# Performance work log

Hardware: AMD Instinct MI355X
Metric: run time of the kernel (lower is better)

## Reference

```python
import jax, jax.numpy as jnp
import numpy as np

VOCAB = 32000
MAXLEN = 512
E = 768
H = 12
D = E // H  # 64
L = 6
F = int(E * 8 / 3)  # 2048
THETA = 10000.0
EPS = 1.1920929e-07  # torch.finfo(float32).eps, RMSNorm default


def _rms_norm(x, w):
    var = jnp.mean(x * x, axis=-1, keepdims=True)
    return x * jax.lax.rsqrt(var + EPS) * w


def _rope(x, cos, sin):
    # x: [B,H,C,D]; cos/sin: [C,D/2] (interleaved even/odd convention)
    xe = x[..., 0::2]
    xo = x[..., 1::2]
    re = xe * cos - xo * sin
    ro = xe * sin + xo * cos
    out = jnp.stack([re, ro], axis=-1)  # [B,H,C,D/2,2]
    return out.reshape(x.shape)


def setup_inputs() -> dict:
    key = jax.random.key(0)
    ks = jax.random.split(key, 13)
    s = 0.02
    ids = jax.random.randint(ks[0], (8, MAXLEN), 0, VOCAB)
    embed = jax.random.normal(ks[1], (VOCAB, E), jnp.float32) * s
    norm1_w = jnp.ones((L, E), jnp.float32)
    wq = jax.random.normal(ks[2], (L, E, H * D), jnp.float32) * s
    wk = jax.random.normal(ks[3], (L, E, H * D), jnp.float32) * s
    wv = jax.random.normal(ks[4], (L, E, H * D), jnp.float32) * s
    wo = jax.random.normal(ks[5], (L, H * D, E), jnp.float32) * s
    norm2_w = jnp.ones((L, E), jnp.float32)
    w_gate = jax.random.normal(ks[6], (L, E, F), jnp.float32) * s
    w_val = jax.random.normal(ks[7], (L, E, F), jnp.float32) * s
    w_out = jax.random.normal(ks[8], (L, F, E), jnp.float32) * s
    normf_w = jnp.ones((E,), jnp.float32)
    unembed = jax.random.normal(ks[9], (E, VOCAB), jnp.float32) * s
    return {"ids": ids, "embed": embed, "norm1_w": norm1_w, "wq": wq,
            "wk": wk, "wv": wv, "wo": wo, "norm2_w": norm2_w,
            "w_gate": w_gate, "w_val": w_val, "w_out": w_out,
            "normf_w": normf_w, "unembed": unembed}


def reference(ids, embed, norm1_w, wq, wk, wv, wo, norm2_w,
              w_gate, w_val, w_out, normf_w, unembed):
    B, C = ids.shape
    # RoPE caches [C, D/2]
    half_ids = jnp.arange(D // 2, dtype=jnp.float32)
    inv_freq = 1.0 / (THETA ** (2.0 * half_ids / D))
    angles = jnp.arange(C, dtype=jnp.float32)[:, None] * inv_freq[None, :]
    cos, sin = jnp.cos(angles), jnp.sin(angles)
    causal = jnp.tril(jnp.ones((C, C), bool))

    x = embed[ids]  # [B,C,E]
    for l in range(L):
        h = _rms_norm(x, norm1_w[l])
        q = (h @ wq[l]).reshape(B, C, H, D).transpose(0, 2, 1, 3)
        k = (h @ wk[l]).reshape(B, C, H, D).transpose(0, 2, 1, 3)
        v = (h @ wv[l]).reshape(B, C, H, D).transpose(0, 2, 1, 3)
        q = _rope(q, cos, sin)
        k = _rope(k, cos, sin)
        scores = jnp.einsum('bhqd,bhkd->bhqk', q, k) / jnp.sqrt(jnp.float32(D))
        scores = jnp.where(causal, scores, -jnp.inf)
        w = jax.nn.softmax(scores, axis=-1)
        attn = jnp.einsum('bhqk,bhkd->bhqd', w, v)
        attn = attn.transpose(0, 2, 1, 3).reshape(B, C, H * D)
        x = x + attn @ wo[l]
        h2 = _rms_norm(x, norm2_w[l])
        gated = jax.nn.silu(h2 @ w_gate[l]) * (h2 @ w_val[l])
        x = x + gated @ w_out[l]
    x = _rms_norm(x, normf_w)
    return x @ unembed  # [B,C,VOCAB]
```

## Files before the change

kernel.cpp:

```cpp
#include <hip/hip_runtime.h>
#include <hip/hip_bf16.h>
#include <stdint.h>

typedef __hip_bfloat16 bf16;
typedef unsigned short ushort_t;
typedef __attribute__((ext_vector_type(8))) short bf16x8;
typedef __attribute__((ext_vector_type(4))) float f32x4;

#define EPSV 1.1920929e-07f

__device__ __forceinline__ float bfu2f(uint32_t u) {
  union { uint32_t i; float f; } t; t.i = u << 16; return t.f;
}
__device__ __forceinline__ ushort_t f2bfu(float f) {
  bf16 h = __float2bfloat16(f);
  return *reinterpret_cast<ushort_t*>(&h);
}

#define BAR() __builtin_amdgcn_s_barrier()
#define SCHEDB() __builtin_amdgcn_sched_barrier(0)
#define WAIT_LGKM0() { asm volatile("s_waitcnt lgkmcnt(0)" ::: "memory"); SCHEDB(); }
#define WAIT_VM4() asm volatile("s_waitcnt vmcnt(4)" ::: "memory")
#define WAIT_VM0() asm volatile("s_waitcnt vmcnt(0)" ::: "memory")

__global__ void rope_table_kernel(float* __restrict__ cosT, float* __restrict__ sinT) {
  int i = blockIdx.x * 256 + threadIdx.x;
  if (i >= 512 * 32) return;
  int c = i >> 5, dp = i & 31;
  float inv = powf(10000.0f, -(2.0f * dp) / 64.0f);
  float a = (float)c * inv;
  cosT[i] = cosf(a);
  sinT[i] = sinf(a);
}

__global__ void embed_kernel(const int* __restrict__ ids, const float* __restrict__ emb,
                             float* __restrict__ x) {
  int t = blockIdx.x;
  int id = ids[t];
  const float4* s = (const float4*)(emb + (size_t)id * 768);
  float4* d = (float4*)(x + (size_t)t * 768);
  d[threadIdx.x] = s[threadIdx.x];
}

__global__ __launch_bounds__(256) void rmsnorm_kernel(const float* __restrict__ x,
                                                      const float* __restrict__ wgt,
                                                      bf16* __restrict__ out) {
  const int row = blockIdx.x;
  const int tid = threadIdx.x;
  const float* xr = x + (size_t)row * 768;
  float v0 = xr[tid], v1 = xr[tid + 256], v2 = xr[tid + 512];
  float s = v0 * v0 + v1 * v1 + v2 * v2;
#pragma unroll
  for (int d = 1; d < 64; d <<= 1) s += __shfl_xor(s, d);
  __shared__ float red[4];
  if ((tid & 63) == 0) red[tid >> 6] = s;
  __syncthreads();
  s = red[0] + red[1] + red[2] + red[3];
  float rs = rsqrtf(s * (1.0f / 768.0f) + EPSV);
  bf16* orow = out + (size_t)row * 768;
  orow[tid]       = __float2bfloat16(v0 * rs * wgt[tid]);
  orow[tid + 256] = __float2bfloat16(v1 * rs * wgt[tid + 256]);
  orow[tid + 512] = __float2bfloat16(v2 * rs * wgt[tid + 512]);
}

__global__ __launch_bounds__(256) void transpose_kernel(const float* __restrict__ in,
                                                        bf16* __restrict__ out,
                                                        int K, int N) {
  __shared__ float tile[32][33];
  int nt = blockIdx.x * 32, kt = blockIdx.y * 32;
  int tx = threadIdx.x & 31, ty = threadIdx.x >> 5;
#pragma unroll
  for (int i = 0; i < 4; ++i)
    tile[ty + i * 8][tx] = in[(size_t)(kt + ty + i * 8) * N + nt + tx];
  __syncthreads();
#pragma unroll
  for (int i = 0; i < 4; ++i)
    out[(size_t)(nt + ty + i * 8) * K + kt + tx] = __float2bfloat16(tile[tx][ty + i * 8]);
}

template <int MODE>
__global__ __launch_bounds__(256) void gemm_bt(const bf16* __restrict__ A,
                                               const bf16* __restrict__ BT,
                                               void* __restrict__ C,
                                               int M, int N, int K) {
  __shared__ __align__(16) bf16 As[128 * 32];
  __shared__ __align__(16) bf16 Bs[128 * 32];
  const int tid = threadIdx.x;
  const int lane = tid & 63, w = tid >> 6;
  const int g = lane >> 4, lc = lane & 15;
  const int bm = blockIdx.y * 128, bn = blockIdx.x * 128;
  const int wm = (w >> 1) * 64, wn = (w & 1) * 64;

  f32x4 acc[4][4];
#pragma unroll
  for (int i = 0; i < 4; ++i)
#pragma unroll
    for (int j = 0; j < 4; ++j) acc[i][j] = (f32x4){0.f, 0.f, 0.f, 0.f};

  for (int k0 = 0; k0 < K; k0 += 32) {
    __syncthreads();
#pragma unroll
    for (int j = 0; j < 2; ++j) {
      int c = (w * 2 + j) * 64 + lane;
      int row = c >> 2, part = c & 3;
      const bf16* srcA = A + (size_t)(bm + row) * K + k0 + part * 8;
      const bf16* srcB = BT + (size_t)(bn + row) * K + k0 + part * 8;
      __builtin_amdgcn_global_load_lds((const __attribute__((address_space(1))) void*)srcA,
                                       (__attribute__((address_space(3))) void*)(As + (w * 2 + j) * 512),
                                       16, 0, 0);
      __builtin_amdgcn_global_load_lds((const __attribute__((address_space(1))) void*)srcB,
                                       (__attribute__((address_space(3))) void*)(Bs + (w * 2 + j) * 512),
                                       16, 0, 0);
    }
    __syncthreads();
    bf16x8 af[4], bfr[4];
#pragma unroll
    for (int mi = 0; mi < 4; ++mi)
      af[mi] = *(const bf16x8*)(As + (wm + mi * 16 + lc) * 32 + g * 8);
#pragma unroll
    for (int ni = 0; ni < 4; ++ni)
      bfr[ni] = *(const bf16x8*)(Bs + (wn + ni * 16 + lc) * 32 + g * 8);
#pragma unroll
    for (int mi = 0; mi < 4; ++mi)
#pragma unroll
      for (int ni = 0; ni < 4; ++ni)
        acc[mi][ni] = __builtin_amdgcn_mfma_f32_16x16x32_bf16(af[mi], bfr[ni], acc[mi][ni], 0, 0, 0);
  }

#pragma unroll
  for (int mi = 0; mi < 4; ++mi)
#pragma unroll
    for (int ni = 0; ni < 4; ++ni)
#pragma unroll
      for (int r = 0; r < 4; ++r) {
        size_t row = (size_t)bm + wm + mi * 16 + g * 4 + r;
        size_t col = (size_t)bn + wn + ni * 16 + lc;
        float v = acc[mi][ni][r];
        if (MODE == 0)      ((bf16*)C)[row * N + col] = __float2bfloat16(v);
        else if (MODE == 1) ((float*)C)[row * N + col] = v;
        else                ((float*)C)[row * N + col] += v;
      }
}

template <int MODE>
__global__ __launch_bounds__(512, 2) void gemm256(const bf16* __restrict__ A,
                                                  const bf16* __restrict__ BT,
                                                  void* __restrict__ C,
                                                  int M, int N, int K) {
  __shared__ __align__(16) bf16 lds[2][4][256 * 32];

  const int tid = threadIdx.x;
  const int lane = tid & 63, w = tid >> 6;
  const int wr = w >> 2, wc = w & 3;
  const int g = lane >> 4, lc = lane & 15;

  const int nwg = gridDim.x;
  const int q = nwg >> 3;
  const int wg = ((int)blockIdx.x & 7) * q + ((int)blockIdx.x >> 3);
  const int nby = M >> 8;
  const int bx = wg / nby, by = wg % nby;
  const int bm = by << 8, bn = bx << 8;

  const bf16* Ap = A + (size_t)bm * K;
  const bf16* Bp = BT + (size_t)bn * K;

  const int soff = (lc * 64) + ((((lane >> 4) ^ ((lane >> 1) & 3)) << 4));

  auto stage_half = [&](int buf, int slab, const bf16* Base, int kcol) {
#pragma unroll
    for (int j = 0; j < 2; ++j) {
      int half_id = w * 2 + j;
      int row = half_id * 16 + (lane >> 2);
      int s_log = (lane & 3) ^ ((lane >> 3) & 3);
      const bf16* src = Base + (size_t)row * K + kcol + s_log * 8;
      bf16* dst = &lds[buf][slab][half_id * 512];
      __builtin_amdgcn_global_load_lds((const __attribute__((address_space(1))) void*)src,
                                       (__attribute__((address_space(3))) void*)dst,
                                       16, 0, 0);
    }
  };

  f32x4 acc[8][4];
#pragma unroll
  for (int i = 0; i < 8; ++i)
#pragma unroll
    for (int j = 0; j < 4; ++j) acc[i][j] = (f32x4){0.f, 0.f, 0.f, 0.f};

  const int NT = K >> 6;

  stage_half(0, 0, Ap, 0);
  stage_half(0, 1, Bp, 0);
  stage_half(0, 2, Ap, 32);
  stage_half(0, 3, Bp, 32);

  bf16x8 aF[4], bF[4];

  auto ds_A = [&](int buf, int kk, int mh) {
#pragma unroll
    for (int i = 0; i < 4; ++i) {
      int byte = (wr * 128 + mh * 64 + i * 16) * 64 + soff;
      aF[i] = *(const bf16x8*)((const char*)&lds[buf][kk * 2][0] + byte);
    }
  };
  auto ds_B = [&](int buf, int kk) {
#pragma unroll
    for (int nf = 0; nf < 4; ++nf) {
      int byte = (wc * 64 + nf * 16) * 64 + soff;
      bF[nf] = *(const bf16x8*)((const char*)&lds[buf][kk * 2 + 1][0] + byte);
    }
  };
  auto mfma16 = [&](int mh) {
    __builtin_amdgcn_s_setprio(1);
#pragma unroll
    for (int i = 0; i < 4; ++i)
#pragma unroll
      for (int nf = 0; nf < 4; ++nf)
        acc[mh * 4 + i][nf] =
            __builtin_amdgcn_mfma_f32_16x16x32_bf16(aF[i], bF[nf], acc[mh * 4 + i][nf], 0, 0, 0);
    __builtin_amdgcn_s_setprio(0);
  };

  for (int t = 0; t < NT; ++t) {
    const int buf = t & 1;
    const bool pf = (t + 1) < NT;
    const int knext = (t + 1) << 6;

    WAIT_VM4();
    BAR(); SCHEDB();
    if (pf) stage_half(buf ^ 1, 0, Ap, knext);
    ds_A(buf, 0, 0);
    ds_B(buf, 0);
    BAR();
    WAIT_LGKM0();
    mfma16(0);
    if (pf) stage_half(buf ^ 1, 1, Bp, knext);
    ds_A(buf, 0, 1);
    BAR();
    WAIT_LGKM0();
    mfma16(1);
    if (pf) { WAIT_VM4(); } else { WAIT_VM0(); }
    BAR(); SCHEDB();
    if (pf) stage_half(buf ^ 1, 2, Ap, knext + 32);
    ds_A(buf, 1, 0);
    ds_B(buf, 1);
    BAR();
    WAIT_LGKM0();
    mfma16(0);
    if (pf) stage_half(buf ^ 1, 3, Bp, knext + 32);
    ds_A(buf, 1, 1);
    BAR();
    WAIT_LGKM0();
    mfma16(1);
  }

#pragma unroll
  for (int mf = 0; mf < 8; ++mf)
#pragma unroll
    for (int nf = 0; nf < 4; ++nf)
#pragma unroll
      for (int r = 0; r < 4; ++r) {
        size_t row = (size_t)bm + wr * 128 + mf * 16 + g * 4 + r;
        size_t col = (size_t)bn + wc * 64 + nf * 16 + lc;
        float v = acc[mf][nf][r];
        if (MODE == 0) ((bf16*)C)[row * N + col] = __float2bfloat16(v);
        else           ((float*)C)[row * N + col] = v;
      }
}

__global__ __launch_bounds__(256) void attn_kernel(const bf16* __restrict__ qkv,
                                                   const float* __restrict__ cosT,
                                                   const float* __restrict__ sinT,
                                                   bf16* __restrict__ out) {
  const int qt = blockIdx.x;
  const int h  = blockIdx.y;
  const int b  = blockIdx.z;
  const int tid = threadIdx.x;
  const int lane = tid & 63, w = tid >> 6;
  const int g = lane >> 4, lc = lane & 15;

  __shared__ __align__(16) bf16 Qs[128][72];
  __shared__ __align__(16) bf16 Ks[64][72];
  __shared__ __align__(16) bf16 Vt[64][72];
  __shared__ __align__(16) bf16 Pl[4][32][72];

  for (int i = 0; i < 16; ++i) {
    int pi = i * 256 + tid;
    int r = pi >> 5, dp = pi & 31;
    int c = qt * 128 + r;
    size_t t = (size_t)b * 512 + c;
    uint32_t u = *(const uint32_t*)(qkv + t * 2304 + h * 64 + dp * 2);
    float xe = bfu2f(u & 0xffffu), xo = bfu2f(u >> 16);
    float cs = cosT[c * 32 + dp], sn = sinT[c * 32 + dp];
    float re = (xe * cs - xo * sn) * 0.125f;
    float ro = (xe * sn + xo * cs) * 0.125f;
    *(uint32_t*)&Qs[r][dp * 2] = (uint32_t)f2bfu(re) | ((uint32_t)f2bfu(ro) << 16);
  }
  __syncthreads();
  bf16x8 qa[2][2];
#pragma unroll
  for (int mi = 0; mi < 2; ++mi)
#pragma unroll
    for (int ks = 0; ks < 2; ++ks)
      qa[mi][ks] = *(const bf16x8*)&Qs[w * 32 + mi * 16 + lc][ks * 32 + g * 8];

  float m_r[2][4], l_r[2][4];
  f32x4 acc_o[2][4];
#pragma unroll
  for (int mi = 0; mi < 2; ++mi)
#pragma unroll
    for (int r = 0; r < 4; ++r) { m_r[mi][r] = -1e30f; l_r[mi][r] = 0.f; }
#pragma unroll
  for (int mi = 0; mi < 2; ++mi)
#pragma unroll
    for (int ni = 0; ni < 4; ++ni) acc_o[mi][ni] = (f32x4){0.f, 0.f, 0.f, 0.f};

  const int nkt = 2 * qt + 2;
  for (int kt = 0; kt < nkt; ++kt) {
    __syncthreads();
    for (int i = 0; i < 8; ++i) {
      int pi = i * 256 + tid;
      int r = pi >> 5, dp = pi & 31;
      int c = kt * 64 + r;
      size_t t = (size_t)b * 512 + c;
      uint32_t u = *(const uint32_t*)(qkv + t * 2304 + 768 + h * 64 + dp * 2);
      float xe = bfu2f(u & 0xffffu), xo = bfu2f(u >> 16);
      float cs = cosT[c * 32 + dp], sn = sinT[c * 32 + dp];
      *(uint32_t*)&Ks[r][dp * 2] =
          (uint32_t)f2bfu(xe * cs - xo * sn) | ((uint32_t)f2bfu(xe * sn + xo * cs) << 16);
      uint32_t uv = *(const uint32_t*)(qkv + t * 2304 + 1536 + h * 64 + dp * 2);
      *(ushort_t*)&Vt[dp * 2][r]     = (ushort_t)(uv & 0xffffu);
      *(ushort_t*)&Vt[dp * 2 + 1][r] = (ushort_t)(uv >> 16);
    }
    __syncthreads();

    f32x4 sacc[2][4];
#pragma unroll
    for (int mi = 0; mi < 2; ++mi)
#pragma unroll
      for (int ni = 0; ni < 4; ++ni) sacc[mi][ni] = (f32x4){0.f, 0.f, 0.f, 0.f};
#pragma unroll
    for (int ni = 0; ni < 4; ++ni) {
      bf16x8 kb0 = *(const bf16x8*)&Ks[ni * 16 + lc][g * 8];
      bf16x8 kb1 = *(const bf16x8*)&Ks[ni * 16 + lc][32 + g * 8];
#pragma unroll
      for (int mi = 0; mi < 2; ++mi) {
        sacc[mi][ni] = __builtin_amdgcn_mfma_f32_16x16x32_bf16(qa[mi][0], kb0, sacc[mi][ni], 0, 0, 0);
        sacc[mi][ni] = __builtin_amdgcn_mfma_f32_16x16x32_bf16(qa[mi][1], kb1, sacc[mi][ni], 0, 0, 0);
      }
    }
    if (kt >= 2 * qt) {
#pragma unroll
      for (int mi = 0; mi < 2; ++mi)
#pragma unroll
        for (int ni = 0; ni < 4; ++ni)
#pragma unroll
          for (int r = 0; r < 4; ++r) {
            int ql = w * 32 + mi * 16 + g * 4 + r;
            int kl = ni * 16 + lc;
            if (kt * 64 + kl > qt * 128 + ql) sacc[mi][ni][r] = -1e30f;
          }
    }
#pragma unroll
    for (int mi = 0; mi < 2; ++mi) {
      float mx[4], sm[4], mn[4], sc[4];
#pragma unroll
      for (int r = 0; r < 4; ++r)
        mx[r] = fmaxf(fmaxf(sacc[mi][0][r], sacc[mi][1][r]), fmaxf(sacc[mi][2][r], sacc[mi][3][r]));
#pragma unroll
      for (int d = 1; d < 16; d <<= 1)
#pragma unroll
        for (int r = 0; r < 4; ++r) mx[r] = fmaxf(mx[r], __shfl_xor(mx[r], d));
#pragma unroll
      for (int r = 0; r < 4; ++r) {
        mn[r] = fmaxf(m_r[mi][r], mx[r]);
        sc[r] = __expf(m_r[mi][r] - mn[r]);
        sm[r] = 0.f;
      }
#pragma unroll
      for (int ni = 0; ni < 4; ++ni)
#pragma unroll
        for (int r = 0; r < 4; ++r) {
          float p = __expf(sacc[mi][ni][r] - mn[r]);
          sacc[mi][ni][r] = p;
          sm[r] += p;
        }
#pragma unroll
      for (int d = 1; d < 16; d <<= 1)
#pragma unroll
        for (int r = 0; r < 4; ++r) sm[r] += __shfl_xor(sm[r], d);
#pragma unroll
      for (int r = 0; r < 4; ++r) {
        l_r[mi][r] = l_r[mi][r] * sc[r] + sm[r];
        m_r[mi][r] = mn[r];
      }
#pragma unroll
      for (int ni = 0; ni < 4; ++ni)
#pragma unroll
        for (int r = 0; r < 4; ++r) acc_o[mi][ni][r] *= sc[r];
#pragma unroll
      for (int ni = 0; ni < 4; ++ni)
#pragma unroll
        for (int r = 0; r < 4; ++r)
          *(ushort_t*)&Pl[w][mi * 16 + g * 4 + r][ni * 16 + lc] = f2bfu(sacc[mi][ni][r]);
    }
    __syncthreads();
#pragma unroll
    for (int ks = 0; ks < 2; ++ks) {
      bf16x8 pa[2];
#pragma unroll
      for (int mi = 0; mi < 2; ++mi)
        pa[mi] = *(const bf16x8*)&Pl[w][mi * 16 + lc][ks * 32 + g * 8];
#pragma unroll
      for (int ni = 0; ni < 4; ++ni) {
        bf16x8 vb = *(const bf16x8*)&Vt[ni * 16 + lc][ks * 32 + g * 8];
#pragma unroll
        for (int mi = 0; mi < 2; ++mi)
          acc_o[mi][ni] = __builtin_amdgcn_mfma_f32_16x16x32_bf16(pa[mi], vb, acc_o[mi][ni], 0, 0, 0);
      }
    }
  }
#pragma unroll
  for (int mi = 0; mi < 2; ++mi) {
    float inv[4];
#pragma unroll
    for (int r = 0; r < 4; ++r) inv[r] = 1.0f / l_r[mi][r];
#pragma unroll
    for (int ni = 0; ni < 4; ++ni)
#pragma unroll
      for (int r = 0; r < 4; ++r) {
        size_t t = (size_t)b * 512 + qt * 128 + w * 32 + mi * 16 + g * 4 + r;
        int d = ni * 16 + lc;
        out[t * 768 + h * 64 + d] = __float2bfloat16(acc_o[mi][ni][r] * inv[r]);
      }
  }
}

__global__ void silu_mul_kernel(const float* __restrict__ gv, bf16* __restrict__ act) {
  size_t i = (size_t)blockIdx.x * 256 + threadIdx.x;
  int t = (int)(i >> 11);
  int j = (int)(i & 2047);
  float gval = gv[(size_t)t * 4096 + j];
  float vval = gv[(size_t)t * 4096 + 2048 + j];
  float sg = gval / (1.0f + __expf(-gval));
  act[i] = __float2bfloat16(sg * vval);
}

extern "C" void kernel_launch(void* const* d_in, const int* in_sizes, int n_in,
                              void* d_out, int out_size, void* d_ws, size_t ws_size,
                              hipStream_t stream) {
  const int*   ids    = (const int*)d_in[0];
  const float* embedW = (const float*)d_in[1];
  const float* norm1w = (const float*)d_in[2];
  const float* wq     = (const float*)d_in[3];
  const float* wk     = (const float*)d_in[4];
  const float* wv     = (const float*)d_in[5];
  const float* wo     = (const float*)d_in[6];
  const float* norm2w = (const float*)d_in[7];
  const float* wgate  = (const float*)d_in[8];
  const float* wval   = (const float*)d_in[9];
  const float* wout   = (const float*)d_in[10];
  const float* normfw = (const float*)d_in[11];
  const float* unemb  = (const float*)d_in[12];

  char* arena = (char*)d_out;
  size_t off = 0;
  auto alloc = [&](size_t bytes) -> char* {
    char* p = arena + off;
    off += (bytes + 255) & ~(size_t)255;
    return p;
  };
  float* x       = (float*)alloc(4096ull * 768 * 4);
  bf16*  h       = (bf16*)alloc(4096ull * 768 * 2);
  bf16*  qkv     = (bf16*)alloc(4096ull * 2304 * 2);
  bf16*  attnout = (bf16*)alloc(4096ull * 768 * 2);
  float* gv      = (float*)alloc(4096ull * 4096 * 4);
  bf16*  act     = (bf16*)alloc(4096ull * 2048 * 2);
  float* cosT    = (float*)alloc(512 * 32 * 4);
  float* sinT    = (float*)alloc(512 * 32 * 4);
  bf16*  wqkvT   = (bf16*)alloc(2304ull * 768 * 2);
  bf16*  woT     = (bf16*)alloc(768ull * 768 * 2);
  bf16*  wgvT    = (bf16*)alloc(4096ull * 768 * 2);
  bf16*  woutT   = (bf16*)alloc(768ull * 2048 * 2);

  bf16* unembT = (bf16*)d_ws;
  bf16* hf     = (bf16*)((char*)d_ws + 32000ull * 768 * 2);

  rope_table_kernel<<<64, 256, 0, stream>>>(cosT, sinT);
  embed_kernel<<<4096, 192, 0, stream>>>(ids, embedW, x);

  for (int l = 0; l < 6; ++l) {
    rmsnorm_kernel<<<4096, 256, 0, stream>>>(x, norm1w + (size_t)l * 768, h);
    transpose_kernel<<<dim3(24, 24), 256, 0, stream>>>(wq + (size_t)l * 768 * 768, wqkvT, 768, 768);
    transpose_kernel<<<dim3(24, 24), 256, 0, stream>>>(wk + (size_t)l * 768 * 768, wqkvT + 768ull * 768, 768, 768);
    transpose_kernel<<<dim3(24, 24), 256, 0, stream>>>(wv + (size_t)l * 768 * 768, wqkvT + 1536ull * 768, 768, 768);
    gemm256<0><<<16 * 9, 512, 0, stream>>>(h, wqkvT, qkv, 4096, 2304, 768);
    attn_kernel<<<dim3(4, 12, 8), 256, 0, stream>>>(qkv, cosT, sinT, attnout);
    transpose_kernel<<<dim3(24, 24), 256, 0, stream>>>(wo + (size_t)l * 768 * 768, woT, 768, 768);
    gemm_bt<2><<<dim3(6, 32), 256, 0, stream>>>(attnout, woT, x, 4096, 768, 768);
    rmsnorm_kernel<<<4096, 256, 0, stream>>>(x, norm2w + (size_t)l * 768, h);
    transpose_kernel<<<dim3(64, 24), 256, 0, stream>>>(wgate + (size_t)l * 768 * 2048, wgvT, 768, 2048);
    transpose_kernel<<<dim3(64, 24), 256, 0, stream>>>(wval + (size_t)l * 768 * 2048, wgvT + 2048ull * 768, 768, 2048);
    gemm256<1><<<16 * 16, 512, 0, stream>>>(h, wgvT, gv, 4096, 4096, 768);
    silu_mul_kernel<<<32768, 256, 0, stream>>>(gv, act);
    transpose_kernel<<<dim3(24, 64), 256, 0, stream>>>(wout + (size_t)l * 2048 * 768, woutT, 2048, 768);
    gemm_bt<2><<<dim3(6, 32), 256, 0, stream>>>(act, woutT, x, 4096, 768, 2048);
  }

  rmsnorm_kernel<<<4096, 256, 0, stream>>>(x, normfw, hf);
  transpose_kernel<<<dim3(1000, 24), 256, 0, stream>>>(unemb, unembT, 768, 32000);
  gemm256<1><<<16 * 125, 512, 0, stream>>>(hf, unembT, (float*)d_out, 4096, 32000, 768);
}
```

Measured before the change: 1.740 ms.

## Batch all weight transposes into one launch and route projections through gemm256

All per-layer weight transpose launches are replaced by a single upfront transpose_all kernel that writes bf16 transposed copies of every layer's weights into enlarged buffers. The output-projection and FFN-down GEMMs move from the 128-tile gemm_bt to the pipelined 256-tile gemm256, which gains an accumulate mode. The gate/value GEMM now writes bf16 instead of fp32, and the SiLU-multiply kernel is vectorized to 8 elements per thread. This removes many small launches and halves intermediate traffic, at the cost of rounding the gate/value outputs to bf16 and launching only 48 blocks for the N=768 GEMMs.

```diff
diff --git a/kernel.cpp b/kernel.cpp
--- a/kernel.cpp
+++ b/kernel.cpp
@@ -63,83 +63,51 @@
   orow[tid + 512] = __float2bfloat16(v2 * rs * wgt[tid + 512]);
 }
 
-__global__ __launch_bounds__(256) void transpose_kernel(const float* __restrict__ in,
-                                                        bf16* __restrict__ out,
-                                                        int K, int N) {
-  __shared__ float tile[32][33];
-  int nt = blockIdx.x * 32, kt = blockIdx.y * 32;
+__global__ __launch_bounds__(256) void transpose_all_kernel(
+    const float* __restrict__ wq, const float* __restrict__ wk,
+    const float* __restrict__ wv, const float* __restrict__ wo,
+    const float* __restrict__ wg, const float* __restrict__ wvl,
+    const float* __restrict__ wout, const float* __restrict__ unemb,
+    bf16* __restrict__ wqkvT, bf16* __restrict__ woT,
+    bf16* __restrict__ wgvT, bf16* __restrict__ woutT,
+    bf16* __restrict__ unembT) {
+  int id = blockIdx.x;
+  const float* src; bf16* dst; int K, N, tile;
+  if (id < 13824) {
+    int m = id / 576; tile = id % 576;
+    int l = m >> 2, w3 = m & 3;
+    K = 768; N = 768;
+    const float* s0 = (w3 == 0) ? wq : (w3 == 1) ? wk : (w3 == 2) ? wv : wo;
+    src = s0 + (size_t)l * 768 * 768;
+    dst = (w3 < 3) ? wqkvT + (size_t)l * 2304 * 768 + (size_t)w3 * 768 * 768
+                   : woT + (size_t)l * 768 * 768;
+  } else if (id < 32256) {
+    int id2 = id - 13824; int m = id2 / 1536; tile = id2 % 1536;
+    int l = m >> 1, w2 = m & 1;
+    K = 768; N = 2048;
+    src = (w2 ? wvl : wg) + (size_t)l * 768 * 2048;
+    dst = wgvT + (size_t)l * 4096 * 768 + (size_t)w2 * 2048 * 768;
+  } else if (id < 41472) {
+    int id2 = id - 32256; int l = id2 / 1536; tile = id2 % 1536;
+    K = 2048; N = 768;
+    src = wout + (size_t)l * 2048 * 768;
+    dst = woutT + (size_t)l * 768 * 2048;
+  } else {
+    tile = id - 41472;
+    K = 768; N = 32000;
+    src = unemb; dst = unembT;
+  }
+  int ntn = N >> 5;
+  int nt = (tile % ntn) << 5, kt = (tile / ntn) << 5;
+  __shared__ float tl[32][33];
   int tx = threadIdx.x & 31, ty = threadIdx.x >> 5;
 #pragma unroll
   for (int i = 0; i < 4; ++i)
-    tile[ty + i * 8][tx] = in[(size_t)(kt + ty + i * 8) * N + nt + tx];
+    tl[ty + i * 8][tx] = src[(size_t)(kt + ty + i * 8) * N + nt + tx];
   __syncthreads();
 #pragma unroll
   for (int i = 0; i < 4; ++i)
-    out[(size_t)(nt + ty + i * 8) * K + kt + tx] = __float2bfloat16(tile[tx][ty + i * 8]);
-}
-
-template <int MODE>
-__global__ __launch_bounds__(256) void gemm_bt(const bf16* __restrict__ A,
-                                               const bf16* __restrict__ BT,
-                                               void* __restrict__ C,
-                                               int M, int N, int K) {
-  __shared__ __align__(16) bf16 As[128 * 32];
-  __shared__ __align__(16) bf16 Bs[128 * 32];
-  const int tid = threadIdx.x;
-  const int lane = tid & 63, w = tid >> 6;
-  const int g = lane >> 4, lc = lane & 15;
-  const int bm = blockIdx.y * 128, bn = blockIdx.x * 128;
-  const int wm = (w >> 1) * 64, wn = (w & 1) * 64;
-
-  f32x4 acc[4][4];
-#pragma unroll
-  for (int i = 0; i < 4; ++i)
-#pragma unroll
-    for (int j = 0; j < 4; ++j) acc[i][j] = (f32x4){0.f, 0.f, 0.f, 0.f};
-
-  for (int k0 = 0; k0 < K; k0 += 32) {
-    __syncthreads();
-#pragma unroll
-    for (int j = 0; j < 2; ++j) {
-      int c = (w * 2 + j) * 64 + lane;
-      int row = c >> 2, part = c & 3;
-      const bf16* srcA = A + (size_t)(bm + row) * K + k0 + part * 8;
-      const bf16* srcB = BT + (size_t)(bn + row) * K + k0 + part * 8;
-      __builtin_amdgcn_global_load_lds((const __attribute__((address_space(1))) void*)srcA,
-                                       (__attribute__((address_space(3))) void*)(As + (w * 2 + j) * 512),
-                                       16, 0, 0);
-      __builtin_amdgcn_global_load_lds((const __attribute__((address_space(1))) void*)srcB,
-                                       (__attribute__((address_space(3))) void*)(Bs + (w * 2 + j) * 512),
-                                       16, 0, 0);
-    }
-    __syncthreads();
-    bf16x8 af[4], bfr[4];
-#pragma unroll
-    for (int mi = 0; mi < 4; ++mi)
-      af[mi] = *(const bf16x8*)(As + (wm + mi * 16 + lc) * 32 + g * 8);
-#pragma unroll
-    for (int ni = 0; ni < 4; ++ni)
-      bfr[ni] = *(const bf16x8*)(Bs + (wn + ni * 16 + lc) * 32 + g * 8);
-#pragma unroll
-    for (int mi = 0; mi < 4; ++mi)
-#pragma unroll
-      for (int ni = 0; ni < 4; ++ni)
-        acc[mi][ni] = __builtin_amdgcn_mfma_f32_16x16x32_bf16(af[mi], bfr[ni], acc[mi][ni], 0, 0, 0);
-  }
-
-#pragma unroll
-  for (int mi = 0; mi < 4; ++mi)
-#pragma unroll
-    for (int ni = 0; ni < 4; ++ni)
-#pragma unroll
-      for (int r = 0; r < 4; ++r) {
-        size_t row = (size_t)bm + wm + mi * 16 + g * 4 + r;
-        size_t col = (size_t)bn + wn + ni * 16 + lc;
-        float v = acc[mi][ni][r];
-        if (MODE == 0)      ((bf16*)C)[row * N + col] = __float2bfloat16(v);
-        else if (MODE == 1) ((float*)C)[row * N + col] = v;
-        else                ((float*)C)[row * N + col] += v;
-      }
+    dst[(size_t)(nt + ty + i * 8) * K + kt + tx] = __float2bfloat16(tl[tx][ty + i * 8]);
 }
 
 template <int MODE>
@@ -233,11 +201,13 @@
     BAR();
     WAIT_LGKM0();
     mfma16(0);
+
     if (pf) stage_half(buf ^ 1, 1, Bp, knext);
     ds_A(buf, 0, 1);
     BAR();
     WAIT_LGKM0();
     mfma16(1);
+
     if (pf) { WAIT_VM4(); } else { WAIT_VM0(); }
     BAR(); SCHEDB();
     if (pf) stage_half(buf ^ 1, 2, Ap, knext + 32);
@@ -246,6 +216,7 @@
     BAR();
     WAIT_LGKM0();
     mfma16(0);
+
     if (pf) stage_half(buf ^ 1, 3, Bp, knext + 32);
     ds_A(buf, 1, 1);
     BAR();
@@ -262,8 +233,9 @@
         size_t row = (size_t)bm + wr * 128 + mf * 16 + g * 4 + r;
         size_t col = (size_t)bn + wc * 64 + nf * 16 + lc;
         float v = acc[mf][nf][r];
-        if (MODE == 0) ((bf16*)C)[row * N + col] = __float2bfloat16(v);
-        else           ((float*)C)[row * N + col] = v;
+        if (MODE == 0)      ((bf16*)C)[row * N + col] = __float2bfloat16(v);
+        else if (MODE == 1) ((float*)C)[row * N + col] = v;
+        else                ((float*)C)[row * N + col] += v;
       }
 }
 
@@ -435,14 +407,20 @@
   }
 }
 
-__global__ void silu_mul_kernel(const float* __restrict__ gv, bf16* __restrict__ act) {
-  size_t i = (size_t)blockIdx.x * 256 + threadIdx.x;
-  int t = (int)(i >> 11);
-  int j = (int)(i & 2047);
-  float gval = gv[(size_t)t * 4096 + j];
-  float vval = gv[(size_t)t * 4096 + 2048 + j];
-  float sg = gval / (1.0f + __expf(-gval));
-  act[i] = __float2bfloat16(sg * vval);
+__global__ void silu_mul_kernel(const bf16* __restrict__ gv, bf16* __restrict__ act) {
+  int c = blockIdx.x * 256 + threadIdx.x;
+  int t = c >> 8, j8 = (c & 255) * 8;
+  bf16x8 gvec = *(const bf16x8*)(gv + (size_t)t * 4096 + j8);
+  bf16x8 vvec = *(const bf16x8*)(gv + (size_t)t * 4096 + 2048 + j8);
+  bf16x8 o;
+#pragma unroll
+  for (int e = 0; e < 8; ++e) {
+    float gval = bfu2f((ushort_t)gvec[e]);
+    float vval = bfu2f((ushort_t)vvec[e]);
+    float sg = gval / (1.0f + __expf(-gval));
+    o[e] = (short)f2bfu(sg * vval);
+  }
+  *(bf16x8*)(act + (size_t)t * 2048 + j8) = o;
 }
 
 extern "C" void kernel_launch(void* const* d_in, const int* in_sizes, int n_in,
@@ -473,40 +451,34 @@
   bf16*  h       = (bf16*)alloc(4096ull * 768 * 2);
   bf16*  qkv     = (bf16*)alloc(4096ull * 2304 * 2);
   bf16*  attnout = (bf16*)alloc(4096ull * 768 * 2);
-  float* gv      = (float*)alloc(4096ull * 4096 * 4);
+  bf16*  gv      = (bf16*)alloc(4096ull * 4096 * 2);
   bf16*  act     = (bf16*)alloc(4096ull * 2048 * 2);
   float* cosT    = (float*)alloc(512 * 32 * 4);
   float* sinT    = (float*)alloc(512 * 32 * 4);
-  bf16*  wqkvT   = (bf16*)alloc(2304ull * 768 * 2);
-  bf16*  woT     = (bf16*)alloc(768ull * 768 * 2);
-  bf16*  wgvT    = (bf16*)alloc(4096ull * 768 * 2);
-  bf16*  woutT   = (bf16*)alloc(768ull * 2048 * 2);
+  bf16*  wqkvT   = (bf16*)alloc(6ull * 2304 * 768 * 2);
+  bf16*  woT     = (bf16*)alloc(6ull * 768 * 768 * 2);
+  bf16*  wgvT    = (bf16*)alloc(6ull * 4096 * 768 * 2);
+  bf16*  woutT   = (bf16*)alloc(6ull * 768 * 2048 * 2);
 
   bf16* unembT = (bf16*)d_ws;
   bf16* hf     = (bf16*)((char*)d_ws + 32000ull * 768 * 2);
 
   rope_table_kernel<<<64, 256, 0, stream>>>(cosT, sinT);
   embed_kernel<<<4096, 192, 0, stream>>>(ids, embedW, x);
+  transpose_all_kernel<<<65472, 256, 0, stream>>>(wq, wk, wv, wo, wgate, wval, wout, unemb,
+                                                  wqkvT, woT, wgvT, woutT, unembT);
 
   for (int l = 0; l < 6; ++l) {
     rmsnorm_kernel<<<4096, 256, 0, stream>>>(x, norm1w + (size_t)l * 768, h);
-    transpose_kernel<<<dim3(24, 24), 256, 0, stream>>>(wq + (size_t)l * 768 * 768, wqkvT, 768, 768);
-    transpose_kernel<<<dim3(24, 24), 256, 0, stream>>>(wk + (size_t)l * 768 * 768, wqkvT + 768ull * 768, 768, 768);
-    transpose_kernel<<<dim3(24, 24), 256, 0, stream>>>(wv + (size_t)l * 768 * 768, wqkvT + 1536ull * 768, 768, 768);
-    gemm256<0><<<16 * 9, 512, 0, stream>>>(h, wqkvT, qkv, 4096, 2304, 768);
+    gemm256<0><<<16 * 9, 512, 0, stream>>>(h, wqkvT + (size_t)l * 2304 * 768, qkv, 4096, 2304, 768);
     attn_kernel<<<dim3(4, 12, 8), 256, 0, stream>>>(qkv, cosT, sinT, attnout);
-    transpose_kernel<<<dim3(24, 24), 256, 0, stream>>>(wo + (size_t)l * 768 * 768, woT, 768, 768);
-    gemm_bt<2><<<dim3(6, 32), 256, 0, stream>>>(attnout, woT, x, 4096, 768, 768);
+    gemm256<2><<<16 * 3, 512, 0, stream>>>(attnout, woT + (size_t)l * 768 * 768, x, 4096, 768, 768);
     rmsnorm_kernel<<<4096, 256, 0, stream>>>(x, norm2w + (size_t)l * 768, h);
-    transpose_kernel<<<dim3(64, 24), 256, 0, stream>>>(wgate + (size_t)l * 768 * 2048, wgvT, 768, 2048);
-    transpose_kernel<<<dim3(64, 24), 256, 0, stream>>>(wval + (size_t)l * 768 * 2048, wgvT + 2048ull * 768, 768, 2048);
-    gemm256<1><<<16 * 16, 512, 0, stream>>>(h, wgvT, gv, 4096, 4096, 768);
-    silu_mul_kernel<<<32768, 256, 0, stream>>>(gv, act);
-    transpose_kernel<<<dim3(24, 64), 256, 0, stream>>>(wout + (size_t)l * 2048 * 768, woutT, 2048, 768);
-    gemm_bt<2><<<dim3(6, 32), 256, 0, stream>>>(act, woutT, x, 4096, 768, 2048);
+    gemm256<0><<<16 * 16, 512, 0, stream>>>(h, wgvT + (size_t)l * 4096 * 768, gv, 4096, 4096, 768);
+    silu_mul_kernel<<<4096, 256, 0, stream>>>(gv, act);
+    gemm256<2><<<16 * 3, 512, 0, stream>>>(act, woutT + (size_t)l * 768 * 2048, x, 4096, 768, 2048);
   }
 
   rmsnorm_kernel<<<4096, 256, 0, stream>>>(x, normfw, hf);
-  transpose_kernel<<<dim3(1000, 24), 256, 0, stream>>>(unemb, unembT, 768, 32000);
   gemm256<1><<<16 * 125, 512, 0, stream>>>(hf, unembT, (float*)d_out, 4096, 32000, 768);
 }
```

After: 1.864 ms. 7.2% more time.
